# Performance work log

Hardware: AMD Instinct MI355X
Metric: run time of the kernel (lower is better)

Reference implementation:

```python
import jax, jax.numpy as jnp
import numpy as np

BRANCH = 8
DEPTH = 4
BATCH = 8192


def _build_tree(b=BRANCH, depth=DEPTH):
    level_sizes = [b ** l for l in range(depth + 1)]
    offsets = np.cumsum([0] + level_sizes)
    E = int(offsets[-1])  # 4681 total nodes (edges)
    parent = np.full(E, -1, dtype=np.int64)
    for l in range(1, depth + 1):
        idx = np.arange(level_sizes[l])
        parent[offsets[l] + idx] = offsets[l - 1] + idx // b
    # Each node's softmax group = its parent's children group; root -> group 0 ('ROOT').
    # Internal nodes occupy indices [0, offsets[depth]), so group id = parent+1.
    seg = np.where(parent < 0, 0, parent + 1).astype(np.int32)
    # path_onehot[i, j] = 1 iff j is an ancestor of i or i itself (path to root)
    P = np.zeros((E, E), dtype=np.float32)
    rows = np.arange(E)
    cur = rows.copy()
    for _ in range(depth + 1):
        P[rows, cur] = 1.0
        cur = np.where(parent[cur] < 0, cur, parent[cur])
    P[rows, cur] = 1.0  # root
    return seg, P


def setup_inputs() -> dict:
    key = jax.random.key(0)
    seg, P = _build_tree()
    E = seg.shape[0]
    inputs = jax.random.normal(key, (BATCH, E), dtype=jnp.float32)
    return {
        "inputs": inputs,
        "segment_ids": jnp.asarray(seg),
        "path_onehot": jnp.asarray(P),
    }


def _cascade_log_softmax(inputs, segment_ids, num_segments):
    # inputs: [B, E]; segmented (per-group) log_softmax along the edge axis.
    xT = inputs.T  # [E, B]
    mx = jax.ops.segment_max(xT, segment_ids, num_segments=num_segments)  # [S, B]
    shifted = xT - mx[segment_ids]
    lse = jnp.log(jax.ops.segment_sum(jnp.exp(shifted), segment_ids,
                                      num_segments=num_segments))  # [S, B]
    return (shifted - lse[segment_ids]).T  # [B, E]


def reference(inputs, segment_ids, path_onehot):
    # final_probabilities: product of conditionals along root-to-node paths
    num_segments = int(jnp.max(segment_ids)) + 1
    log_prob = _cascade_log_softmax(inputs, segment_ids, num_segments)  # [B, E]
    # log p(node) = sum of conditional log-probs over ancestors-or-self
    return jnp.exp(log_prob @ path_onehot.T)  # [B, E]
```

## Files before the change

kernel.cpp:

```cpp
#include <hip/hip_runtime.h>


constexpr int E  = 4681;
constexpr int NG = 585;

template<int S>
__device__ __forceinline__ void loadL(const float* __restrict__ rin, int g, float L[12]) {
    if (g == 584) {
        #pragma unroll
        for (int t = 0; t < 8; ++t) L[S + t] = rin[4673 + t];
        return;
    }
    const float* ap = rin + 8 * g + 1 - S;
    const float4 A = *(const float4*)ap;
    const float4 B = *(const float4*)(ap + 4);
    L[0] = A.x; L[1] = A.y; L[2] = A.z; L[3] = A.w;
    L[4] = B.x; L[5] = B.y; L[6] = B.z; L[7] = B.w;
    if (S != 0) {
        const float4 C = *(const float4*)(ap + 8);
        L[8] = C.x; L[9] = C.y; L[10] = C.z; L[11] = C.w;
    }
}

template<int S>
__device__ __forceinline__ float group_adj(const float L[12]) {
    float m = L[S];
    #pragma unroll
    for (int t = 1; t < 8; ++t) m = fmaxf(m, L[S + t]);
    float s = 0.0f;
    #pragma unroll
    for (int t = 0; t < 8; ++t) s += __expf(L[S + t] - m);
    return -m - __logf(s);
}

template<int S>
__device__ __forceinline__ void store8(float* __restrict__ q, const float L[12], float D) {
    float y[8];
    #pragma unroll
    for (int t = 0; t < 8; ++t) y[t] = __expf(L[S + t] + D);
    if (S == 0) {
        *(float4*)(q)     = make_float4(y[0], y[1], y[2], y[3]);
        *(float4*)(q + 4) = make_float4(y[4], y[5], y[6], y[7]);
    } else if (S == 1) {
        q[0] = y[0];
        *(float2*)(q + 1) = make_float2(y[1], y[2]);
        *(float4*)(q + 3) = make_float4(y[3], y[4], y[5], y[6]);
        q[7] = y[7];
    } else if (S == 2) {
        *(float2*)(q)     = make_float2(y[0], y[1]);
        *(float4*)(q + 2) = make_float4(y[2], y[3], y[4], y[5]);
        *(float2*)(q + 6) = make_float2(y[6], y[7]);
    } else {
        q[0] = y[0];
        *(float4*)(q + 1) = make_float4(y[1], y[2], y[3], y[4]);
        *(float2*)(q + 5) = make_float2(y[5], y[6]);
        q[7] = y[7];
    }
}

template<int S>
__device__ __forceinline__ void row_body(const float* __restrict__ rin,
                                         float* __restrict__ rout,
                                         float* adj, int tid) {
    const int g0 = tid, g1 = tid + 256, g2 = tid + 512;
    const bool h2 = (g2 < NG);

    float L0[12], L1[12], L2[12];
    loadL<S>(rin, g0, L0);
    loadL<S>(rin, g1, L1);

    const int p0   = (g0 - 1) >> 3;
    const int pc0  = p0 < 0 ? 0 : p0;
    const int pp0  = (pc0 - 1) >> 3;
    const int ppc0 = pp0 < 0 ? 0 : pp0;
    const float xg0 = rin[g0], xp0 = rin[pc0], xpp0 = rin[ppc0];

    const int p1 = (g1 - 1) >> 3, pp1 = (p1 - 1) >> 3;
    const float xg1 = rin[g1], xp1 = rin[p1], xpp1 = rin[pp1];

    int p2 = 0, pp2 = 0;
    float xg2 = 0.f, xp2 = 0.f, xpp2 = 0.f;
    if (h2) {
        loadL<S>(rin, g2, L2);
        p2 = (g2 - 1) >> 3; pp2 = (p2 - 1) >> 3;
        xg2 = rin[g2]; xp2 = rin[p2]; xpp2 = rin[pp2];
    }
    __builtin_amdgcn_sched_barrier(0);

    const float adj0 = group_adj<S>(L0);
    const float adj1 = group_adj<S>(L1);
    adj[g0] = adj0;
    adj[g1] = adj1;
    float adj2 = 0.f;
    if (h2) { adj2 = group_adj<S>(L2); adj[g2] = adj2; }
    __syncthreads();

    const float a00 = adj[0];
    const float a10 = adj[pc0], a20 = adj[ppc0];
    float D0 = adj0;
    if (g0 > 0) {
        D0 += xg0 + a10;
        if (p0 > 0) {
            D0 += xp0 + a20;
            if (pp0 > 0) D0 += xpp0 + a00;
        }
    }
    const float D1 = adj1 + xg1 + adj[p1] + xp1 + adj[pp1] + xpp1 + a00;

    store8<S>(rout + 8 * g0 + 1, L0, D0);
    store8<S>(rout + 8 * g1 + 1, L1, D1);
    if (h2) {
        const float D2 = adj2 + xg2 + adj[p2] + xp2 + adj[pp2] + xpp2 + a00;
        store8<S>(rout + 8 * g2 + 1, L2, D2);
    }
    if (tid == 0) rout[0] = 1.0f;
}

__global__ __launch_bounds__(256, 8) void cascade_kernel(const float* __restrict__ in,
                                                         float* __restrict__ out) {
    __shared__ float adj[NG];
    const int tid = threadIdx.x;
    const long long rowbase = (long long)blockIdx.x * (long long)E;
    const float* rin = in + rowbase;
    float* rout = out + rowbase;
    switch ((int)((rowbase + 1) & 3)) {
        case 0: row_body<0>(rin, rout, adj, tid); break;
        case 1: row_body<1>(rin, rout, adj, tid); break;
        case 2: row_body<2>(rin, rout, adj, tid); break;
        case 3: row_body<3>(rin, rout, adj, tid); break;
    }
}

extern "C" void kernel_launch(void* const* d_in, const int* in_sizes, int n_in,
                              void* d_out, int out_size, void* d_ws, size_t ws_size,
                              hipStream_t stream) {
    const float* in = (const float*)d_in[0];
    float* out = (float*)d_out;
    const int B = in_sizes[0] / E;
    cascade_kernel<<<B, 256, 0, stream>>>(in, out);
}
```

Baseline: 305.2 us.

## Stage whole row into padded LDS via async global_load_lds

Instead of each thread loading its 8-wide windows into registers with unaligned vector loads plus scattered ancestor reads, the whole input row is copied into LDS with global_load_lds, using a 9-stride padded layout. The padding slot of each group holds the group's adjustment term, so one buffer serves both the inputs and the adj values. Ancestor walks and exponentials then read from LDS. This removes the redundant and misaligned global reads, but the loads become 4-byte-per-lane async copies, there is a full wait before any compute, LDS use grows to about 21KB per block, and the launch-bounds occupancy hint drops from 8 to 7.

```diff
diff --git a/kernel.cpp b/kernel.cpp
--- a/kernel.cpp
+++ b/kernel.cpp
@@ -1,43 +1,60 @@
 #include <hip/hip_runtime.h>
 
 
-constexpr int E  = 4681;
-constexpr int NG = 585;
+constexpr int E     = 4681;
+constexpr int NG    = 585;
+constexpr int NSLOT = 5266;
 
-template<int S>
-__device__ __forceinline__ void loadL(const float* __restrict__ rin, int g, float L[12]) {
-    if (g == 584) {
-        #pragma unroll
-        for (int t = 0; t < 8; ++t) L[S + t] = rin[4673 + t];
-        return;
+__device__ __forceinline__ int xslot(int i) { return 9 * (i >> 3) + (i & 7); }
+
+__device__ __forceinline__ void async_ld(const float* g, float* l) {
+    __builtin_amdgcn_global_load_lds(
+        (const __attribute__((address_space(1))) void*)g,
+        (__attribute__((address_space(3))) void*)l, 4, 0, 0);
+}
+
+__device__ __forceinline__ float group_adj(const float w[8]) {
+    float m = w[0];
+    #pragma unroll
+    for (int k = 1; k < 8; ++k) m = fmaxf(m, w[k]);
+    float s = 0.0f;
+    #pragma unroll
+    for (int k = 0; k < 8; ++k) s += __expf(w[k] - m);
+    return -m - __logf(s);
+}
+
+__device__ __forceinline__ void rdwin(const float* xs, int g, float w[8]) {
+    const float* b = xs + 9 * g;
+    #pragma unroll
+    for (int k = 0; k < 7; ++k) w[k] = b[1 + k];
+    w[7] = b[9];
+}
+
+__device__ __forceinline__ float walkD(const float* xs, int g, float adjv) {
+    float D = adjv;
+    if (g > 0) {
+        const int p = (g - 1) >> 3;
+        D += xs[xslot(g)] + xs[9 * p + 8];
+        if (p > 0) {
+            const int pp = (p - 1) >> 3;
+            D += xs[xslot(p)] + xs[9 * pp + 8];
+            if (pp > 0) D += xs[xslot(pp)] + xs[8];
+        }
     }
-    const float* ap = rin + 8 * g + 1 - S;
-    const float4 A = *(const float4*)ap;
-    const float4 B = *(const float4*)(ap + 4);
-    L[0] = A.x; L[1] = A.y; L[2] = A.z; L[3] = A.w;
-    L[4] = B.x; L[5] = B.y; L[6] = B.z; L[7] = B.w;
-    if (S != 0) {
-        const float4 C = *(const float4*)(ap + 8);
-        L[8] = C.x; L[9] = C.y; L[10] = C.z; L[11] = C.w;
-    }
+    return D;
 }
 
 template<int S>
-__device__ __forceinline__ float group_adj(const float L[12]) {
-    float m = L[S];
-    #pragma unroll
-    for (int t = 1; t < 8; ++t) m = fmaxf(m, L[S + t]);
-    float s = 0.0f;
-    #pragma unroll
-    for (int t = 0; t < 8; ++t) s += __expf(L[S + t] - m);
-    return -m - __logf(s);
-}
-
-template<int S>
-__device__ __forceinline__ void store8(float* __restrict__ q, const float L[12], float D) {
+__device__ __forceinline__ void emit(float* __restrict__ rout, const float* xs,
+                                     int g, float D) {
     float y[8];
-    #pragma unroll
-    for (int t = 0; t < 8; ++t) y[t] = __expf(L[S + t] + D);
+    {
+        const float* b = xs + 9 * g;
+        #pragma unroll
+        for (int k = 0; k < 7; ++k) y[k] = __expf(b[1 + k] + D);
+        y[7] = __expf(b[9] + D);
+    }
+    float* q = rout + 8 * g + 1;
     if (S == 0) {
         *(float4*)(q)     = make_float4(y[0], y[1], y[2], y[3]);
         *(float4*)(q + 4) = make_float4(y[4], y[5], y[6], y[7]);
@@ -61,73 +78,50 @@
 template<int S>
 __device__ __forceinline__ void row_body(const float* __restrict__ rin,
                                          float* __restrict__ rout,
-                                         float* adj, int tid) {
+                                         float* xs, int tid) {
+    const int lbase = tid & ~63;
+    #pragma unroll
+    for (int j = 0; j < 21; ++j) {
+        const int s = 256 * j + tid;
+        if (s < NSLOT && (s % 9) != 8) {
+            async_ld(rin + 8 * (s / 9) + (s % 9), xs + 256 * j + lbase);
+        }
+    }
+    asm volatile("s_waitcnt vmcnt(0)" ::: "memory");
+    __syncthreads();
+
     const int g0 = tid, g1 = tid + 256, g2 = tid + 512;
     const bool h2 = (g2 < NG);
-
-    float L0[12], L1[12], L2[12];
-    loadL<S>(rin, g0, L0);
-    loadL<S>(rin, g1, L1);
-
-    const int p0   = (g0 - 1) >> 3;
-    const int pc0  = p0 < 0 ? 0 : p0;
-    const int pp0  = (pc0 - 1) >> 3;
-    const int ppc0 = pp0 < 0 ? 0 : pp0;
-    const float xg0 = rin[g0], xp0 = rin[pc0], xpp0 = rin[ppc0];
-
-    const int p1 = (g1 - 1) >> 3, pp1 = (p1 - 1) >> 3;
-    const float xg1 = rin[g1], xp1 = rin[p1], xpp1 = rin[pp1];
-
-    int p2 = 0, pp2 = 0;
-    float xg2 = 0.f, xp2 = 0.f, xpp2 = 0.f;
-    if (h2) {
-        loadL<S>(rin, g2, L2);
-        p2 = (g2 - 1) >> 3; pp2 = (p2 - 1) >> 3;
-        xg2 = rin[g2]; xp2 = rin[p2]; xpp2 = rin[pp2];
-    }
-    __builtin_amdgcn_sched_barrier(0);
-
-    const float adj0 = group_adj<S>(L0);
-    const float adj1 = group_adj<S>(L1);
-    adj[g0] = adj0;
-    adj[g1] = adj1;
-    float adj2 = 0.f;
-    if (h2) { adj2 = group_adj<S>(L2); adj[g2] = adj2; }
+    float w[8];
+    rdwin(xs, g0, w);
+    const float a0 = group_adj(w);
+    rdwin(xs, g1, w);
+    const float a1 = group_adj(w);
+    float a2 = 0.f;
+    if (h2) { rdwin(xs, g2, w); a2 = group_adj(w); }
+    xs[9 * g0 + 8] = a0;
+    xs[9 * g1 + 8] = a1;
+    if (h2) xs[9 * g2 + 8] = a2;
     __syncthreads();
 
-    const float a00 = adj[0];
-    const float a10 = adj[pc0], a20 = adj[ppc0];
-    float D0 = adj0;
-    if (g0 > 0) {
-        D0 += xg0 + a10;
-        if (p0 > 0) {
-            D0 += xp0 + a20;
-            if (pp0 > 0) D0 += xpp0 + a00;
-        }
-    }
-    const float D1 = adj1 + xg1 + adj[p1] + xp1 + adj[pp1] + xpp1 + a00;
-
-    store8<S>(rout + 8 * g0 + 1, L0, D0);
-    store8<S>(rout + 8 * g1 + 1, L1, D1);
-    if (h2) {
-        const float D2 = adj2 + xg2 + adj[p2] + xp2 + adj[pp2] + xpp2 + a00;
-        store8<S>(rout + 8 * g2 + 1, L2, D2);
-    }
+    emit<S>(rout, xs, g0, walkD(xs, g0, a0));
+    emit<S>(rout, xs, g1, walkD(xs, g1, a1));
+    if (h2) emit<S>(rout, xs, g2, walkD(xs, g2, a2));
     if (tid == 0) rout[0] = 1.0f;
 }
 
-__global__ __launch_bounds__(256, 8) void cascade_kernel(const float* __restrict__ in,
+__global__ __launch_bounds__(256, 7) void cascade_kernel(const float* __restrict__ in,
                                                          float* __restrict__ out) {
-    __shared__ float adj[NG];
+    __shared__ float xs[NSLOT];
     const int tid = threadIdx.x;
     const long long rowbase = (long long)blockIdx.x * (long long)E;
     const float* rin = in + rowbase;
     float* rout = out + rowbase;
     switch ((int)((rowbase + 1) & 3)) {
-        case 0: row_body<0>(rin, rout, adj, tid); break;
-        case 1: row_body<1>(rin, rout, adj, tid); break;
-        case 2: row_body<2>(rin, rout, adj, tid); break;
-        case 3: row_body<3>(rin, rout, adj, tid); break;
+        case 0: row_body<0>(rin, rout, xs, tid); break;
+        case 1: row_body<1>(rin, rout, xs, tid); break;
+        case 2: row_body<2>(rin, rout, xs, tid); break;
+        case 3: row_body<3>(rin, rout, xs, tid); break;
     }
 }
 
```

Result: faster. 297.2 us (-2.6%).
